# Kernel optimization log

Hardware: AMD Instinct MI355X
Metric: run time of the kernel (lower is better)

Reference implementation:

```python
import jax, jax.numpy as jnp
import numpy as np
import math

N_HEADS = 12


def setup_inputs() -> dict:
    key = jax.random.key(0)
    ks = jax.random.split(key, 6)
    B, S, DIM = 4, 2048, 768
    h = jax.random.normal(ks[0], (B, S, DIM), dtype=jnp.float32)
    attn_mask = jnp.ones((B, 1, 1, S), dtype=jnp.int32)
    scale = 1.0 / math.sqrt(DIM)
    wq = jax.random.normal(ks[1], (DIM, DIM), dtype=jnp.float32) * scale
    wk = jax.random.normal(ks[2], (DIM, DIM), dtype=jnp.float32) * scale
    wv = jax.random.normal(ks[3], (DIM, DIM), dtype=jnp.float32) * scale
    wo = jax.random.normal(ks[4], (DIM, DIM), dtype=jnp.float32) * scale
    return {"h": h, "attn_mask": attn_mask, "wq": wq, "wk": wk, "wv": wv, "wo": wo}


def reference(h, attn_mask, wq, wk, wv, wo):
    B, S, dim = h.shape
    H = N_HEADS
    D = dim // H
    qk_scale = 1.0 / math.sqrt(D)
    # NOTE: original uses .view(B, H, S, D) on the [B, S, H*D] projection —
    # a raw reshape, NOT the usual (B,S,H,D)->(B,H,S,D) transpose. Reproduce exactly.
    hq = (h @ wq.T).reshape(B, H, S, D)
    hk = (h @ wk.T).reshape(B, H, S, D)
    hv = (h @ wv.T).reshape(B, H, S, D)
    scores = jnp.einsum("bhqd,bhkd->bhqk", hq, hk) * qk_scale  # [B,H,S,S]
    scores = jnp.where(attn_mask == 0, -jnp.inf, scores)
    attn = jax.nn.softmax(scores.astype(jnp.float32), axis=-1)
    ctx = jnp.einsum("bhqk,bhkd->bhqd", attn, hv)  # [B,H,S,D]
    # dropout is identity in eval mode
    ctx = ctx.reshape(B, S, H * D)
    return ctx @ wo.T
```

## Files before the change

### kernel.cpp

```cpp
#include <hip/hip_runtime.h>
#include <math.h>

typedef __bf16 bf16x8 __attribute__((ext_vector_type(8)));
typedef float  f32x4  __attribute__((ext_vector_type(4)));
typedef float  f32x16 __attribute__((ext_vector_type(16)));

#define MFMA16(a, b, c) __builtin_amdgcn_mfma_f32_16x16x32_bf16((a), (b), (c), 0, 0, 0)
#define MFMA32(a, b, c) __builtin_amdgcn_mfma_f32_32x32x16_bf16((a), (b), (c), 0, 0, 0)

__device__ __forceinline__ unsigned short f2bf(float f) {
    unsigned int u = __float_as_uint(f);
    u += 0x7fffu + ((u >> 16) & 1u);
    return (unsigned short)(u >> 16);
}

__device__ __forceinline__ void gll16(const unsigned short* g, unsigned short* l) {
    __builtin_amdgcn_global_load_lds(
        (const __attribute__((address_space(1))) unsigned int*)g,
        (__attribute__((address_space(3))) unsigned int*)l, 16, 0, 0);
}

__global__ __launch_bounds__(256) void convert_kernel(
    const float* __restrict__ h, const float* __restrict__ wq,
    const float* __restrict__ wk, const float* __restrict__ wv,
    const float* __restrict__ wo,
    unsigned short* __restrict__ hb, unsigned short* __restrict__ wb)
{
    const int NH4 = 1572864;
    const int NW4 = 147456;
    int i4 = blockIdx.x * 256 + threadIdx.x;
    const float4* src;
    unsigned short* dst;
    int off;
    float sc = 1.0f;
    if (i4 < NH4) {
        src = (const float4*)h; dst = hb; off = i4;
    } else {
        int j = i4 - NH4;
        int w = j / NW4;
        off = j - w * NW4;
        const float* s = (w == 0) ? wq : (w == 1) ? wk : (w == 2) ? wv : wo;
        if (w == 0) sc = 0.18033688011112042f;
        src = (const float4*)s;
        dst = wb + w * 589824;
    }
    float4 v = src[off];
    ushort4 o;
    o.x = f2bf(v.x * sc); o.y = f2bf(v.y * sc);
    o.z = f2bf(v.z * sc); o.w = f2bf(v.w * sc);
    ((ushort4*)dst)[off] = o;
}

template <typename OutT>
__global__ __launch_bounds__(256) void gemm_bt(
    const unsigned short* __restrict__ A,
    const unsigned short* __restrict__ Bm,
    OutT* __restrict__ C)
{
    constexpr int K = 768, N = 768;
    __shared__ unsigned short As[2][128 * 32];
    __shared__ unsigned short Bs[2][128 * 32];
    const unsigned short* Bz = Bm + (size_t)blockIdx.z * N * K;
    OutT* Cz = C + (size_t)blockIdx.z * 8192 * N;

    const int tid  = threadIdx.x;
    const int bm   = blockIdx.x * 128, bn = blockIdx.y * 128;
    const int wave = tid >> 6, lane = tid & 63;
    const int wm   = (wave & 1) * 64, wn = (wave >> 1) * 64;
    const int l16  = lane & 15, quad = lane >> 4;

    const int sr  = tid >> 2;
    const int sp8 = ((tid & 3) ^ (sr & 3)) * 8;
    const int slot8 = (quad ^ (l16 & 3)) * 8;

    auto stage = [&](int k0, int bi) {
        gll16(A  + (size_t)(bm + sr) * K      + k0 + sp8, As[bi] + tid * 8);
        gll16(A  + (size_t)(bm + 64 + sr) * K + k0 + sp8, As[bi] + 2048 + tid * 8);
        gll16(Bz + (size_t)(bn + sr) * K      + k0 + sp8, Bs[bi] + tid * 8);
        gll16(Bz + (size_t)(bn + 64 + sr) * K + k0 + sp8, Bs[bi] + 2048 + tid * 8);
    };

    f32x4 acc[4][4] = {};

    stage(0, 0);
    __syncthreads();

    for (int i = 0; i < 24; i++) {
        const int cur = i & 1;
        if (i < 23) stage((i + 1) * 32, cur ^ 1);

        bf16x8 af[4], bfv[4];
        #pragma unroll
        for (int ii = 0; ii < 4; ii++)
            af[ii] = *(const bf16x8*)(As[cur] + (wm + ii * 16 + l16) * 32 + slot8);
        #pragma unroll
        for (int jj = 0; jj < 4; jj++)
            bfv[jj] = *(const bf16x8*)(Bs[cur] + (wn + jj * 16 + l16) * 32 + slot8);
        #pragma unroll
        for (int ii = 0; ii < 4; ii++)
            #pragma unroll
            for (int jj = 0; jj < 4; jj++)
                acc[ii][jj] = MFMA16(af[ii], bfv[jj], acc[ii][jj]);

        __syncthreads();
    }

    #pragma unroll
    for (int ii = 0; ii < 4; ii++) {
        #pragma unroll
        for (int jj = 0; jj < 4; jj++) {
            int row0 = bm + wm + ii * 16 + quad * 4;
            int col  = bn + wn + jj * 16 + l16;
            #pragma unroll
            for (int r = 0; r < 4; r++) {
                float v = acc[ii][jj][r];
                size_t idx = (size_t)(row0 + r) * N + col;
                if constexpr (sizeof(OutT) == 2) Cz[idx] = f2bf(v);
                else                             Cz[idx] = v;
            }
        }
    }
}

__global__ __launch_bounds__(256) void vtrans_kernel(
    const unsigned short* __restrict__ Vg,
    unsigned short* __restrict__ vt)
{
    constexpr int LDT = 72;
    __shared__ unsigned short Ts[64 * LDT];
    const int b = blockIdx.z, hh = blockIdx.y, kp0 = blockIdx.x * 64;
    const int tid = threadIdx.x;
    const size_t boff = (size_t)b * (24576 * 64);
    const int rowV0 = hh * 2048 + kp0;

    #pragma unroll
    for (int rep = 0; rep < 2; rep++) {
        int idx = rep * 256 + tid;
        int r = idx >> 3, dp = (idx & 7) * 8;
        uint4 v = *(const uint4*)(Vg + boff + (size_t)(rowV0 + r) * 64 + dp);
        unsigned short tmp[8];
        *(uint4*)tmp = v;
        #pragma unroll
        for (int i = 0; i < 8; i++) Ts[(dp + i) * LDT + r] = tmp[i];
    }
    __syncthreads();
    unsigned short* vtb = vt + ((size_t)(b * 12 + hh)) * 64 * 2048;
    #pragma unroll
    for (int rep = 0; rep < 2; rep++) {
        int idx = rep * 256 + tid;
        int d = idx >> 3, kp = (idx & 7) * 8;
        uint4 v = *(const uint4*)(Ts + d * LDT + kp);
        *(uint4*)(vtb + (size_t)d * 2048 + kp0 + kp) = v;
    }
}

__global__ __launch_bounds__(256) void attn_kernel(
    const unsigned short* __restrict__ Qg,
    const unsigned short* __restrict__ Kg,
    const unsigned short* __restrict__ vt,
    const int* __restrict__ mask,
    unsigned short* __restrict__ Og)
{
    __shared__ unsigned short Qs[128 * 64];
    __shared__ unsigned short Ks[2][64 * 64];
    __shared__ unsigned short Vs[2][64 * 64];
    __shared__ unsigned long long msh[32];

    const int b = blockIdx.z, hh = blockIdx.y, qt = blockIdx.x;
    const int tid  = threadIdx.x;
    const int wave = tid >> 6, lane = tid & 63;
    const int c31  = lane & 31, h = lane >> 5;
    const size_t boff = (size_t)b * (24576 * 64);
    const int rowQ0 = hh * 2048 + qt * 128;
    const int rowK0 = hh * 2048;
    const unsigned short* vtg = vt + ((size_t)(b * 12 + hh)) * 64 * 2048;
    const int sw = c31 & 7;

    const int srow = tid >> 3;
    const int sch8 = ((tid & 7) ^ (srow & 7)) * 8;

    auto stageKV = [&](int kt, int bi) {
        #pragma unroll
        for (int i = 0; i < 2; i++) {
            int row = i * 32 + srow;
            gll16(Kg  + boff + (size_t)(rowK0 + kt * 64 + row) * 64 + sch8,
                  Ks[bi] + i * 2048 + tid * 8);
            gll16(vtg + (size_t)row * 2048 + kt * 64 + sch8,
                  Vs[bi] + i * 2048 + tid * 8);
        }
    };

    #pragma unroll
    for (int i = 0; i < 4; i++) {
        int row = i * 32 + srow;
        gll16(Qg + boff + (size_t)(rowQ0 + row) * 64 + sch8, Qs + i * 2048 + tid * 8);
    }
    stageKV(0, 0);

    {
        const int4 a = *(const int4*)(mask + b * 2048 + tid * 8);
        const int4 c = *(const int4*)(mask + b * 2048 + tid * 8 + 4);
        unsigned char byte =
            (a.x != 0 ? 1u : 0u)       | (a.y != 0 ? 2u : 0u) |
            (a.z != 0 ? 4u : 0u)       | (a.w != 0 ? 8u : 0u) |
            (c.x != 0 ? 16u : 0u)      | (c.y != 0 ? 32u : 0u) |
            (c.z != 0 ? 64u : 0u)      | (c.w != 0 ? 128u : 0u);
        ((unsigned char*)msh)[tid] = byte;
    }
    __syncthreads();

    bf16x8 qf[4];
    #pragma unroll
    for (int c = 0; c < 4; c++) {
        int ch = (2 * c + h) ^ sw;
        qf[c] = *(const bf16x8*)(Qs + (wave * 32 + c31) * 64 + ch * 8);
    }

    f32x16 acc[2] = {};
    f32x16 acc_l  = {};
    bf16x8 onesf;
    #pragma unroll
    for (int i = 0; i < 8; i++) onesf[i] = (__bf16)1.0f;

    for (int kt = 0; kt < 32; kt++) {
        const int cur = kt & 1;
        if (kt < 31) stageKV(kt + 1, cur ^ 1);

        const unsigned long long am = msh[kt];

        f32x16 sT[2];
        #pragma unroll
        for (int t2 = 0; t2 < 2; t2++) {
            f32x16 z = {};
            #pragma unroll
            for (int c = 0; c < 4; c++) {
                int ch = (2 * c + h) ^ sw;
                bf16x8 kf = *(const bf16x8*)(Ks[cur] + (t2 * 32 + c31) * 64 + ch * 8);
                z = MFMA32(kf, qf[c], z);
            }
            sT[t2] = z;
        }

        unsigned int p01[2][4], p23[2][4];
        if (am == ~0ull) {
            #pragma unroll
            for (int t2 = 0; t2 < 2; t2++) {
                #pragma unroll
                for (int s = 0; s < 4; s++) {
                    float e0 = __builtin_amdgcn_exp2f(sT[t2][4*s+0]);
                    float e1 = __builtin_amdgcn_exp2f(sT[t2][4*s+1]);
                    float e2 = __builtin_amdgcn_exp2f(sT[t2][4*s+2]);
                    float e3 = __builtin_amdgcn_exp2f(sT[t2][4*s+3]);
                    asm("v_cvt_pk_bf16_f32 %0, %1, %2"
                        : "=v"(p01[t2][s]) : "v"(e0), "v"(e1));
                    asm("v_cvt_pk_bf16_f32 %0, %1, %2"
                        : "=v"(p23[t2][s]) : "v"(e2), "v"(e3));
                }
            }
        } else {
            #pragma unroll
            for (int t2 = 0; t2 < 2; t2++) {
                #pragma unroll
                for (int s = 0; s < 4; s++) {
                    unsigned int nib = (unsigned int)(am >> (t2 * 32 + 8 * s + 4 * h)) & 0xFu;
                    float e0 = __builtin_amdgcn_exp2f(sT[t2][4*s+0]);
                    float e1 = __builtin_amdgcn_exp2f(sT[t2][4*s+1]);
                    float e2 = __builtin_amdgcn_exp2f(sT[t2][4*s+2]);
                    float e3 = __builtin_amdgcn_exp2f(sT[t2][4*s+3]);
                    e0 = (nib & 1u) ? e0 : 0.f;
                    e1 = (nib & 2u) ? e1 : 0.f;
                    e2 = (nib & 4u) ? e2 : 0.f;
                    e3 = (nib & 8u) ? e3 : 0.f;
                    asm("v_cvt_pk_bf16_f32 %0, %1, %2"
                        : "=v"(p01[t2][s]) : "v"(e0), "v"(e1));
                    asm("v_cvt_pk_bf16_f32 %0, %1, %2"
                        : "=v"(p23[t2][s]) : "v"(e2), "v"(e3));
                }
            }
        }

        #pragma unroll
        for (int q = 0; q < 4; q++) {
            int t = q >> 1, p = q & 1;
            unsigned int a01 = p01[t][2 * p], b01 = p01[t][2 * p + 1];
            unsigned int a23 = p23[t][2 * p], b23 = p23[t][2 * p + 1];
            asm("v_permlane32_swap_b32 %0, %1" : "+v"(a01), "+v"(b01));
            asm("v_permlane32_swap_b32 %0, %1" : "+v"(a23), "+v"(b23));
            uint4 pfu;
            pfu.x = a01;
            pfu.y = a23;
            pfu.z = b01;
            pfu.w = b23;
            bf16x8 pf;
            __builtin_memcpy(&pf, &pfu, 16);
            #pragma unroll
            for (int nt = 0; nt < 2; nt++) {
                int ch = (2 * q + h) ^ sw;
                bf16x8 vf = *(const bf16x8*)(Vs[cur] + (nt * 32 + c31) * 64 + ch * 8);
                acc[nt] = MFMA32(pf, vf, acc[nt]);
            }
            acc_l = MFMA32(pf, onesf, acc_l);
        }

        __syncthreads();
    }

    #pragma unroll
    for (int reg = 0; reg < 16; reg++) {
        int rowfn = (reg & 3) + 8 * (reg >> 2) + 4 * h;
        float li = __builtin_amdgcn_rcpf(acc_l[reg]);
        int row = rowQ0 + wave * 32 + rowfn;
        #pragma unroll
        for (int nt = 0; nt < 2; nt++)
            Og[boff + (size_t)row * 64 + nt * 32 + c31] = f2bf(acc[nt][reg] * li);
    }
}

extern "C" void kernel_launch(void* const* d_in, const int* in_sizes, int n_in,
                              void* d_out, int out_size, void* d_ws, size_t ws_size,
                              hipStream_t stream)
{
    const float* h    = (const float*)d_in[0];
    const int*   mask = (const int*)d_in[1];
    const float* wq   = (const float*)d_in[2];
    const float* wk   = (const float*)d_in[3];
    const float* wv   = (const float*)d_in[4];
    const float* wo   = (const float*)d_in[5];

    unsigned short* hb  = (unsigned short*)d_ws;
    unsigned short* wb  = hb + 6291456;
    unsigned short* qkv = wb + 4 * 589824;
    unsigned short* ctx = qkv + (size_t)3 * 6291456;

    convert_kernel<<<8448, 256, 0, stream>>>(h, wq, wk, wv, wo, hb, wb);
    gemm_bt<unsigned short><<<dim3(64, 6, 3), 256, 0, stream>>>(hb, wb, qkv);
    vtrans_kernel<<<dim3(32, 12, 4), 256, 0, stream>>>(qkv + (size_t)2 * 6291456, hb);
    attn_kernel<<<dim3(16, 12, 4), 256, 0, stream>>>(
        qkv, qkv + 6291456, hb, mask, ctx);
    gemm_bt<float><<<dim3(64, 6, 1), 256, 0, stream>>>(
        ctx, wb + (size_t)3 * 589824, (float*)d_out);
}
```

Measured before the change: 258.2 us.

## Triple-buffer K/V tiles with one barrier per iteration and load Q directly into registers

Switches the attention kernel's K/V staging from double to triple buffering, prefetching two tiles ahead. Each iteration now waits only on the older loads via an explicit vmcnt wait plus barrier, and the trailing barrier is removed. Q fragments are read straight from global memory into registers instead of through LDS, which frees the LDS that pays for the third buffer. This lets global-to-LDS loads overlap more with MFMA work, at the cost of hand-written waitcnt logic that depends on the exact number of outstanding loads and on uncoalesced direct Q reads.

```diff
diff --git a/kernel.cpp b/kernel.cpp
--- a/kernel.cpp
+++ b/kernel.cpp
@@ -161,9 +161,8 @@
     const int* __restrict__ mask,
     unsigned short* __restrict__ Og)
 {
-    __shared__ unsigned short Qs[128 * 64];
-    __shared__ unsigned short Ks[2][64 * 64];
-    __shared__ unsigned short Vs[2][64 * 64];
+    __shared__ unsigned short Ks[3 * 4096];
+    __shared__ unsigned short Vs[3 * 4096];
     __shared__ unsigned long long msh[32];
 
     const int b = blockIdx.z, hh = blockIdx.y, qt = blockIdx.x;
@@ -184,18 +183,20 @@
         for (int i = 0; i < 2; i++) {
             int row = i * 32 + srow;
             gll16(Kg  + boff + (size_t)(rowK0 + kt * 64 + row) * 64 + sch8,
-                  Ks[bi] + i * 2048 + tid * 8);
+                  Ks + bi * 4096 + i * 2048 + tid * 8);
             gll16(vtg + (size_t)row * 2048 + kt * 64 + sch8,
-                  Vs[bi] + i * 2048 + tid * 8);
+                  Vs + bi * 4096 + i * 2048 + tid * 8);
         }
     };
 
-    #pragma unroll
-    for (int i = 0; i < 4; i++) {
-        int row = i * 32 + srow;
-        gll16(Qg + boff + (size_t)(rowQ0 + row) * 64 + sch8, Qs + i * 2048 + tid * 8);
-    }
-    stageKV(0, 0);
+    bf16x8 qf[4];
+    {
+        const unsigned short* qrow =
+            Qg + boff + (size_t)(rowQ0 + wave * 32 + c31) * 64;
+        #pragma unroll
+        for (int c = 0; c < 4; c++)
+            qf[c] = *(const bf16x8*)(qrow + (2 * c + h) * 8);
+    }
 
     {
         const int4 a = *(const int4*)(mask + b * 2048 + tid * 8);
@@ -209,12 +210,8 @@
     }
     __syncthreads();
 
-    bf16x8 qf[4];
-    #pragma unroll
-    for (int c = 0; c < 4; c++) {
-        int ch = (2 * c + h) ^ sw;
-        qf[c] = *(const bf16x8*)(Qs + (wave * 32 + c31) * 64 + ch * 8);
-    }
+    stageKV(0, 0);
+    stageKV(1, 1);
 
     f32x16 acc[2] = {};
     f32x16 acc_l  = {};
@@ -222,11 +219,20 @@
     #pragma unroll
     for (int i = 0; i < 8; i++) onesf[i] = (__bf16)1.0f;
 
+    int cur = 0;
     for (int kt = 0; kt < 32; kt++) {
-        const int cur = kt & 1;
-        if (kt < 31) stageKV(kt + 1, cur ^ 1);
+        if (kt < 31) asm volatile("s_waitcnt vmcnt(4)\n\ts_barrier" ::: "memory");
+        else         asm volatile("s_waitcnt vmcnt(0)\n\ts_barrier" ::: "memory");
+        __builtin_amdgcn_sched_barrier(0);
+
+        if (kt < 30) {
+            int nb = cur + 2; if (nb >= 3) nb -= 3;
+            stageKV(kt + 2, nb);
+        }
 
         const unsigned long long am = msh[kt];
+        const unsigned short* Kc = Ks + cur * 4096;
+        const unsigned short* Vc = Vs + cur * 4096;
 
         f32x16 sT[2];
         #pragma unroll
@@ -235,7 +241,7 @@
             #pragma unroll
             for (int c = 0; c < 4; c++) {
                 int ch = (2 * c + h) ^ sw;
-                bf16x8 kf = *(const bf16x8*)(Ks[cur] + (t2 * 32 + c31) * 64 + ch * 8);
+                bf16x8 kf = *(const bf16x8*)(Kc + (t2 * 32 + c31) * 64 + ch * 8);
                 z = MFMA32(kf, qf[c], z);
             }
             sT[t2] = z;
@@ -296,13 +302,13 @@
             #pragma unroll
             for (int nt = 0; nt < 2; nt++) {
                 int ch = (2 * q + h) ^ sw;
-                bf16x8 vf = *(const bf16x8*)(Vs[cur] + (nt * 32 + c31) * 64 + ch * 8);
+                bf16x8 vf = *(const bf16x8*)(Vc + (nt * 32 + c31) * 64 + ch * 8);
                 acc[nt] = MFMA32(pf, vf, acc[nt]);
             }
             acc_l = MFMA32(pf, onesf, acc_l);
         }
 
-        __syncthreads();
+        cur = (cur == 2) ? 0 : cur + 1;
     }
 
     #pragma unroll
```

Result: faster. 253.1 us (-2.0%).
